# Kernel optimization log

Measured on AMD Instinct MI355X. Metric: run time of the kernel, lower is better.

The kernel has to match this reference:

```python
import jax, jax.numpy as jnp
import numpy as np

N, L, F, C, H, QK, Vd, Pq, Pv = 1, 512, 128, 64, 12, 32, 32, 8, 8


def _l2g(R, t, p):
    # p: (N,L,...,3) local -> global: R @ p + t
    o = jnp.einsum('nlij,nl...j->nl...i', R, p)
    return o + t.reshape(t.shape[0], t.shape[1], *((1,) * (p.ndim - 3)), 3)


def _g2l(R, t, q):
    # global -> local: R^T (q - t)
    d = q - t.reshape(t.shape[0], t.shape[1], *((1,) * (q.ndim - 3)), 3)
    return jnp.einsum('nlij,nl...i->nl...j', R, d)


def _ln(y, s, b, eps=1e-5):
    mu = y.mean(-1, keepdims=True)
    var = ((y - mu) ** 2).mean(-1, keepdims=True)
    return (y - mu) / jnp.sqrt(var + eps) * s + b


def setup_inputs() -> dict:
    key = jax.random.key(0)
    ks = jax.random.split(key, 16)
    sF = 1.0 / np.sqrt(F)
    sC = 1.0 / np.sqrt(C)
    cat = H * C + H * Vd + H * Pv * 3
    return {
        'R': jax.random.normal(ks[0], (N, L, 3, 3), jnp.float32),
        't': jax.random.normal(ks[1], (N, L, 3), jnp.float32),
        'x': jax.random.normal(ks[2], (N, L, F), jnp.float32),
        'z': jax.random.normal(ks[3], (N, L, L, C), jnp.float32),
        'mask': jnp.ones((N, L), dtype=bool),
        'Wq': jax.random.normal(ks[4], (F, H * QK), jnp.float32) * sF,
        'Wk': jax.random.normal(ks[5], (F, H * QK), jnp.float32) * sF,
        'Wpair': jax.random.normal(ks[6], (C, H), jnp.float32) * sC,
        'Wqp': jax.random.normal(ks[7], (F, H * Pq * 3), jnp.float32) * sF,
        'Wkp': jax.random.normal(ks[8], (F, H * Pq * 3), jnp.float32) * sF,
        'Wv': jax.random.normal(ks[9], (F, H * Vd), jnp.float32) * sF,
        'Wvp': jax.random.normal(ks[10], (F, H * Pv * 3), jnp.float32) * sF,
        'spatial_coef': jnp.full((1, 1, 1, H), np.log(np.e - 1.0), jnp.float32),
        'Wo': jax.random.normal(ks[11], (cat, F), jnp.float32) / np.sqrt(cat),
        'bo': jnp.zeros((F,), jnp.float32),
        'ln1_scale': jnp.ones((F,), jnp.float32),
        'ln1_offset': jnp.zeros((F,), jnp.float32),
        'W1': jax.random.normal(ks[12], (F, F), jnp.float32) * sF,
        'b1': jnp.zeros((F,), jnp.float32),
        'W2': jax.random.normal(ks[13], (F, F), jnp.float32) * sF,
        'b2': jnp.zeros((F,), jnp.float32),
        'W3': jax.random.normal(ks[14], (F, F), jnp.float32) * sF,
        'b3': jnp.zeros((F,), jnp.float32),
        'ln2_scale': jnp.ones((F,), jnp.float32),
        'ln2_offset': jnp.zeros((F,), jnp.float32),
    }


def reference(R, t, x, z, mask, Wq, Wk, Wpair, Wqp, Wkp, Wv, Wvp, spatial_coef,
              Wo, bo, ln1_scale, ln1_offset, W1, b1, W2, b2, W3, b3,
              ln2_scale, ln2_offset):
    # --- node logits ---
    q = (x @ Wq).reshape(N, L, H, QK)
    k = (x @ Wk).reshape(N, L, H, QK)
    logits_node = jnp.einsum('nihd,njhd->nijh', q, k) / np.float32(np.sqrt(QK))
    # --- pair logits ---
    logits_pair = z @ Wpair  # (N,L,L,H)
    # --- spatial logits ---
    qp = _l2g(R, t, (x @ Wqp).reshape(N, L, H * Pq, 3)).reshape(N, L, H, Pq * 3)
    kp = _l2g(R, t, (x @ Wkp).reshape(N, L, H * Pq, 3)).reshape(N, L, H, Pq * 3)
    q2 = (qp ** 2).sum(-1)  # (N,L,H)
    k2 = (kp ** 2).sum(-1)
    sum_sq_dist = q2[:, :, None] + k2[:, None] - 2.0 * jnp.einsum('nihd,njhd->nijh', qp, kp)
    gamma = jax.nn.softplus(spatial_coef)  # (1,1,1,H)
    logits_spatial = sum_sq_dist * (-gamma * np.float32(np.sqrt(2.0 / (9 * Pq))) / 2.0)
    # --- combine, mask, softmax ---
    logits = (logits_node + logits_pair + logits_spatial) * np.float32(np.sqrt(1.0 / 3.0))
    mask_pair = mask[:, :, None] & mask[:, None, :]  # (N,L,L)
    logits = jnp.where(mask_pair[..., None], logits, logits - 100000.0)
    alpha = jax.nn.softmax(logits, axis=2)
    alpha = jnp.where(mask[:, :, None, None], alpha, 0.0)
    # --- pair aggregation ---
    feat_p2n = jnp.einsum('nijh,nijc->nihc', alpha, z).reshape(N, L, H * C)
    # --- node aggregation ---
    v = (x @ Wv).reshape(N, L, H, Vd)
    feat_node = jnp.einsum('nijh,njhd->nihd', alpha, v).reshape(N, L, H * Vd)
    # --- spatial aggregation ---
    vp = _l2g(R, t, (x @ Wvp).reshape(N, L, H, Pv, 3))  # (N,L,H,Pv,3)
    aggr = jnp.einsum('nijh,njhpd->nihpd', alpha, vp)
    feat_points = _g2l(R, t, aggr)
    feat_spatial = feat_points.reshape(N, L, H * Pv * 3)
    # --- output transform + residual/LN + MLP ---
    feat_all = jnp.concatenate([feat_p2n, feat_node, feat_spatial], axis=-1) @ Wo + bo
    feat_all = jnp.where(mask[..., None], feat_all, 0.0)
    x1 = _ln(x + feat_all, ln1_scale, ln1_offset)
    h = jax.nn.relu(x1 @ W1 + b1)
    h = jax.nn.relu(h @ W2 + b2)
    mlp = h @ W3 + b3
    return _ln(x1 + mlp, ln2_scale, ln2_offset)
```

## Files before the change

kernel.cpp:

```cpp
#include <hip/hip_runtime.h>

#define PCOLS 2016

constexpr float INV_SQRT_QK = 0.17677669529663687f;
constexpr float S3          = 0.57735026918962576f;

#define FMA4(acc, s, b) { acc.x += (s)*(b).x; acc.y += (s)*(b).y; acc.z += (s)*(b).z; acc.w += (s)*(b).w; }
#define ADD4(acc, b)    { acc.x += (b).x; acc.y += (b).y; acc.z += (b).z; acc.w += (b).w; }

__global__ __launch_bounds__(384) void k1_gemm(
    const float* __restrict__ x,
    const float* __restrict__ Wq, const float* __restrict__ Wk,
    const float* __restrict__ Wqp, const float* __restrict__ Wkp,
    const float* __restrict__ Wv, const float* __restrict__ Wvp,
    float* __restrict__ proj) {
  int bt = blockIdx.x;
  int it = bt / 21, ot = bt % 21;
  int i0 = it * 64;
  int tid = threadIdx.x;
  __shared__ float xs[64 * 128];
  __shared__ float ws[128 * 96];
  const float* Wsec; int lofs, width;
  if (ot < 4)       { Wsec = Wq;  lofs = ot * 96;        width = 384; }
  else if (ot < 8)  { Wsec = Wk;  lofs = (ot - 4) * 96;  width = 384; }
  else if (ot < 11) { Wsec = Wqp; lofs = (ot - 8) * 96;  width = 288; }
  else if (ot < 14) { Wsec = Wkp; lofs = (ot - 11) * 96; width = 288; }
  else if (ot < 18) { Wsec = Wv;  lofs = (ot - 14) * 96; width = 384; }
  else              { Wsec = Wvp; lofs = (ot - 18) * 96; width = 288; }
  for (int g = tid; g < 2048; g += 384)
    *(float4*)(xs + (g >> 5) * 128 + (g & 31) * 4) =
      *(const float4*)(x + (size_t)(i0 + (g >> 5)) * 128 + (g & 31) * 4);
  for (int g = tid; g < 3072; g += 384) {
    int r = g / 24, u = g % 24;
    *(float4*)(ws + r * 96 + u * 4) = *(const float4*)(Wsec + (size_t)r * width + lofs + u * 4);
  }
  __syncthreads();
  int cg = tid % 24, tr = tid / 24;
  float4 acc0 = {0,0,0,0}, acc1 = {0,0,0,0}, acc2 = {0,0,0,0}, acc3 = {0,0,0,0};
  const float* x0 = xs + (tr * 4 + 0) * 128;
  const float* x1 = xs + (tr * 4 + 1) * 128;
  const float* x2 = xs + (tr * 4 + 2) * 128;
  const float* x3 = xs + (tr * 4 + 3) * 128;
  #pragma unroll 4
  for (int k = 0; k < 128; ++k) {
    float4 w = *(const float4*)(ws + k * 96 + cg * 4);
    FMA4(acc0, x0[k], w); FMA4(acc1, x1[k], w);
    FMA4(acc2, x2[k], w); FMA4(acc3, x3[k], w);
  }
  int gc = ot * 96 + cg * 4;
  *(float4*)(proj + (size_t)(i0 + tr * 4 + 0) * PCOLS + gc) = acc0;
  *(float4*)(proj + (size_t)(i0 + tr * 4 + 1) * PCOLS + gc) = acc1;
  *(float4*)(proj + (size_t)(i0 + tr * 4 + 2) * PCOLS + gc) = acc2;
  *(float4*)(proj + (size_t)(i0 + tr * 4 + 3) * PCOLS + gc) = acc3;
}

__global__ __launch_bounds__(256) void k1b_prep(
    const float* __restrict__ Rg, const float* __restrict__ tg, const float* __restrict__ sc,
    float* __restrict__ proj, float* __restrict__ Ac, float* __restrict__ BcT,
    float* __restrict__ a2, float* __restrict__ b2) {
  int j = blockIdx.x, tid = threadIdx.x;
  __shared__ float qk[1344];
  __shared__ float vps[288], Rs[9], ts[3], cf[12];
  float* pr = proj + (size_t)j * PCOLS;
  const float4* pr4 = (const float4*)pr;
  for (int g = tid; g < 336; g += 256) ((float4*)qk)[g] = pr4[g];
  for (int g = tid; g < 72; g += 256) ((float4*)vps)[g] = pr4[432 + g];
  if (tid < 9) Rs[tid] = Rg[j * 9 + tid];
  else if (tid < 12) ts[tid - 9] = tg[j * 3 + tid - 9];
  else if (tid < 24) cf[tid - 12] = -log1pf(__expf(sc[tid - 12])) * (1.0f / 12.0f);
  __syncthreads();
  for (int p = tid; p < 288; p += 256) {
    int sec = p / 96, m = p % 96;
    float* P = (sec == 0) ? qk + 768 : (sec == 1) ? qk + 1056 : vps;
    float* pp = P + m * 3;
    float p0 = pp[0], p1 = pp[1], p2 = pp[2];
    pp[0] = Rs[0]*p0 + Rs[1]*p1 + Rs[2]*p2 + ts[0];
    pp[1] = Rs[3]*p0 + Rs[4]*p1 + Rs[5]*p2 + ts[1];
    pp[2] = Rs[6]*p0 + Rs[7]*p1 + Rs[8]*p2 + ts[2];
  }
  __syncthreads();
  for (int g = tid; g < 72; g += 256) ((float4*)pr)[432 + g] = ((float4*)vps)[g];
  if (tid < 24) {
    int h = tid % 12;
    const float* s = (tid < 12) ? qk + 768 + h * 24 : qk + 1056 + h * 24;
    float a = 0.f;
    #pragma unroll
    for (int d = 0; d < 24; ++d) a += s[d] * s[d];
    float val = S3 * cf[h] * a;
    if (tid < 12) a2[h * 512 + j] = val; else b2[h * 512 + j] = val;
  }
  float s1 = S3 * INV_SQRT_QK;
  for (int o = tid; o < 672; o += 256) {
    int h = o / 56, d = o % 56;
    float s2 = -2.0f * S3 * cf[h];
    float aval = (d < 32) ? qk[h * 32 + d] * s1 : qk[768 + h * 24 + (d - 32)] * s2;
    float bval = (d < 32) ? qk[384 + h * 32 + d] : qk[1056 + h * 24 + (d - 32)];
    Ac[((size_t)h * 512 + j) * 56 + d] = aval;
    BcT[((size_t)h * 56 + d) * 512 + j] = bval;
  }
}

__global__ __launch_bounds__(256) void k2a_pair(
    const float* __restrict__ z, const float* __restrict__ Wpair,
    float* __restrict__ alphab) {
  int blk = blockIdx.x;
  int i = blk >> 2, j0 = (blk & 3) * 128;
  int tid = threadIdx.x;
  __shared__ float zt[128 * 68];
  __shared__ float wp[768];
  __shared__ float pl[12 * 128];
  if (tid < 192) ((float4*)wp)[tid] = ((const float4*)Wpair)[tid];
  const float4* zsrc = (const float4*)(z + ((size_t)i * 512 + j0) * 64);
  for (int g = tid; g < 2048; g += 256) {
    int row = g >> 4, c4 = g & 15;
    ((float4*)(zt + row * 68))[c4] = zsrc[row * 16 + c4];
  }
  __syncthreads();
  int jl = tid & 127, half = tid >> 7;
  float acc[12];
  #pragma unroll
  for (int h = 0; h < 12; ++h) acc[h] = 0.f;
  const float4* zr = (const float4*)(zt + jl * 68) + half * 8;
  #pragma unroll
  for (int c4 = 0; c4 < 8; ++c4) {
    float4 zv = zr[c4];
    const float* w0 = wp + (half * 8 + c4) * 48;
    #pragma unroll
    for (int h = 0; h < 12; ++h)
      acc[h] += zv.x * w0[h] + zv.y * w0[12 + h] + zv.z * w0[24 + h] + zv.w * w0[36 + h];
  }
  if (half == 1) {
    #pragma unroll
    for (int h = 0; h < 12; ++h) pl[h * 128 + jl] = acc[h];
  }
  __syncthreads();
  if (half == 0) {
    #pragma unroll
    for (int h = 0; h < 12; ++h)
      alphab[(size_t)h * 262144 + (size_t)i * 512 + j0 + jl] = (acc[h] + pl[h * 128 + jl]) * S3;
  }
}

__global__ __launch_bounds__(256) void k2b_logits(
    const float* __restrict__ Ac, const float* __restrict__ BcT,
    const float* __restrict__ a2, const float* __restrict__ b2,
    const float* __restrict__ proj, const float* __restrict__ Rg, const float* __restrict__ tg,
    float* __restrict__ alphab, float* __restrict__ featb) {
  int blk = blockIdx.x;
  int h = blk >> 5, i0 = (blk & 31) * 16;
  int tid = threadIdx.x;
  int ti = tid >> 5, tj = tid & 31;
  int r0 = 2 * ti;
  __shared__ float smem[12480];
  float* At  = smem;
  float* BtT = smem + 960;
  float* b2s = smem + 8352;
  float* a2s = smem + 8864;
  float* als = smem;
  float* Bt  = smem + 8256;
  float* ag  = smem + 12096;
  for (int g = tid; g < 224; g += 256) {
    int row = g / 14, u = g % 14;
    *(float4*)(At + row * 60 + u * 4) =
      *(const float4*)(Ac + ((size_t)h * 512 + i0 + row) * 56 + u * 4);
  }
  if (tid < 128) ((float4*)b2s)[tid] = ((const float4*)(b2 + h * 512))[tid];
  if (tid < 16) a2s[tid] = a2[h * 512 + i0 + tid];
  float lg[2][16];
  const size_t abase = (size_t)h * 262144;
  for (int jt = 0; jt < 4; ++jt) {
    int j0 = jt * 128;
    __syncthreads();
    for (int g = tid; g < 1792; g += 256) {
      int k = g >> 5, c4 = g & 31;
      *(float4*)(BtT + k * 132 + c4 * 4) =
        *(const float4*)(BcT + ((size_t)h * 56 + k) * 512 + j0 + c4 * 4);
    }
    __syncthreads();
    float acc[2][4] = {{0.f,0.f,0.f,0.f},{0.f,0.f,0.f,0.f}};
    #pragma unroll 8
    for (int k = 0; k < 56; ++k) {
      float a0 = At[r0 * 60 + k], a1 = At[(r0 + 1) * 60 + k];
      float2 bA = *(const float2*)(BtT + k * 132 + 2 * tj);
      float2 bB = *(const float2*)(BtT + k * 132 + 64 + 2 * tj);
      acc[0][0] += a0 * bA.x; acc[0][1] += a0 * bA.y; acc[0][2] += a0 * bB.x; acc[0][3] += a0 * bB.y;
      acc[1][0] += a1 * bA.x; acc[1][1] += a1 * bA.y; acc[1][2] += a1 * bB.x; acc[1][3] += a1 * bB.y;
    }
    #pragma unroll
    for (int r = 0; r < 2; ++r) {
      int ig = i0 + r0 + r;
      const float* prow = alphab + abase + (size_t)ig * 512 + j0;
      int c0 = 2 * tj, c1 = 64 + 2 * tj;
      float arr = a2s[r0 + r];
      lg[r][jt*4+0] = acc[r][0] + prow[c0]     + arr + b2s[j0 + c0];
      lg[r][jt*4+1] = acc[r][1] + prow[c0 + 1] + arr + b2s[j0 + c0 + 1];
      lg[r][jt*4+2] = acc[r][2] + prow[c1]     + arr + b2s[j0 + c1];
      lg[r][jt*4+3] = acc[r][3] + prow[c1 + 1] + arr + b2s[j0 + c1 + 1];
    }
  }
  __syncthreads();
  #pragma unroll
  for (int r = 0; r < 2; ++r) {
    float m = lg[r][0];
    #pragma unroll
    for (int u = 1; u < 16; ++u) m = fmaxf(m, lg[r][u]);
    #pragma unroll
    for (int s = 16; s > 0; s >>= 1) m = fmaxf(m, __shfl_xor(m, s));
    float ssum = 0.f;
    #pragma unroll
    for (int u = 0; u < 16; ++u) { lg[r][u] = __expf(lg[r][u] - m); ssum += lg[r][u]; }
    #pragma unroll
    for (int s = 16; s > 0; s >>= 1) ssum += __shfl_xor(ssum, s);
    float inv = 1.0f / ssum;
    int row = r0 + r;
    float* orow = alphab + abase + (size_t)(i0 + row) * 512;
    #pragma unroll
    for (int jt = 0; jt < 4; ++jt) {
      float2 vA = make_float2(lg[r][jt*4+0] * inv, lg[r][jt*4+1] * inv);
      float2 vB = make_float2(lg[r][jt*4+2] * inv, lg[r][jt*4+3] * inv);
      *(float2*)(orow + jt * 128 + 2 * tj)      = vA;
      *(float2*)(orow + jt * 128 + 64 + 2 * tj) = vB;
      *(float2*)(als + row * 516 + jt * 128 + 2 * tj)      = vA;
      *(float2*)(als + row * 516 + jt * 128 + 64 + 2 * tj) = vB;
    }
  }
  int cg2 = tid % 14, rg = tid / 14;
  int c0 = cg2 * 4;
  float4 acc4 = {0,0,0,0};
  for (int t8 = 0; t8 < 8; ++t8) {
    int j0 = t8 * 64;
    __syncthreads();
    for (int g = tid; g < 896; g += 256) {
      int row = g / 14, u = g % 14;
      const float* pr = proj + (size_t)(j0 + row) * PCOLS;
      float4 vv = (u < 8) ? *(const float4*)(&pr[1344 + h * 32 + u * 4])
                          : *(const float4*)(&pr[1728 + h * 24 + (u - 8) * 4]);
      int dst = (u < 8) ? u * 4 : 32 + (u - 8) * 4;
      *(float4*)(Bt + row * 60 + dst) = vv;
    }
    __syncthreads();
    if (rg < 16) {
      const float* arow = als + rg * 516 + j0;
      #pragma unroll 8
      for (int kk = 0; kk < 64; ++kk) {
        float a = arow[kk];
        float4 b = *(const float4*)(Bt + kk * 60 + c0);
        FMA4(acc4, a, b);
      }
    }
  }
  __syncthreads();
  if (rg < 16) {
    if (c0 < 32) {
      *(float4*)(&featb[(size_t)(i0 + rg) * 1440 + 768 + h * 32 + c0]) = acc4;
    } else {
      int cc = c0 - 32;
      ag[rg * 24 + cc + 0] = acc4.x; ag[rg * 24 + cc + 1] = acc4.y;
      ag[rg * 24 + cc + 2] = acc4.z; ag[rg * 24 + cc + 3] = acc4.w;
    }
  }
  __syncthreads();
  if (tid < 128) {
    int row = tid >> 3, p = tid & 7;
    const float* R  = Rg + (size_t)(i0 + row) * 9;
    const float* tt = tg + (size_t)(i0 + row) * 3;
    float d0 = ag[row * 24 + p * 3 + 0] - tt[0];
    float d1 = ag[row * 24 + p * 3 + 1] - tt[1];
    float d2 = ag[row * 24 + p * 3 + 2] - tt[2];
    float* o = featb + (size_t)(i0 + row) * 1440 + 1152 + h * 24 + p * 3;
    o[0] = R[0]*d0 + R[3]*d1 + R[6]*d2;
    o[1] = R[1]*d0 + R[4]*d1 + R[7]*d2;
    o[2] = R[2]*d0 + R[5]*d1 + R[8]*d2;
  }
}

__global__ __launch_bounds__(256) void k3a_p2n(
    const float* __restrict__ alphab, const float* __restrict__ z,
    float* __restrict__ featb) {
  int i = blockIdx.x, tid = threadIdx.x;
  __shared__ float al[12 * 516];
  __shared__ float zt[64 * 68];
  for (int g = tid; g < 1536; g += 256) {
    int row = g >> 7, c4 = g & 127;
    *(float4*)(al + row * 516 + c4 * 4) =
      *(const float4*)(alphab + (size_t)row * 262144 + (size_t)i * 512 + c4 * 4);
  }
  int h = tid >> 4, c4 = tid & 15;
  float4 acc = {0.f, 0.f, 0.f, 0.f};
  const float4* zsrc = (const float4*)(z + (size_t)i * 512 * 64);
  for (int t8 = 0; t8 < 8; ++t8) {
    __syncthreads();
    for (int g = tid; g < 1024; g += 256) {
      int row = g >> 4, cc = g & 15;
      *(float4*)(&zt[row * 68 + cc * 4]) = zsrc[(t8 * 64 + row) * 16 + cc];
    }
    __syncthreads();
    if (tid < 192) {
      const float* ar = al + h * 516 + t8 * 64;
      #pragma unroll
      for (int k4 = 0; k4 < 16; ++k4) {
        float4 a4 = *(const float4*)(&ar[k4 * 4]);
        float4 z0 = *(const float4*)(&zt[(k4*4+0) * 68 + c4 * 4]);
        float4 z1 = *(const float4*)(&zt[(k4*4+1) * 68 + c4 * 4]);
        float4 z2 = *(const float4*)(&zt[(k4*4+2) * 68 + c4 * 4]);
        float4 z3 = *(const float4*)(&zt[(k4*4+3) * 68 + c4 * 4]);
        FMA4(acc, a4.x, z0); FMA4(acc, a4.y, z1); FMA4(acc, a4.z, z2); FMA4(acc, a4.w, z3);
      }
    }
  }
  if (tid < 192)
    *(float4*)(&featb[(size_t)i * 1440 + h * 64 + c4 * 4]) = acc;
}

__global__ __launch_bounds__(512) void k4_mlp(
    const float* __restrict__ featb, const float* __restrict__ x,
    const float* __restrict__ Wo, const float* __restrict__ bo,
    const float* __restrict__ ln1s, const float* __restrict__ ln1o,
    const float* __restrict__ W1, const float* __restrict__ b1,
    const float* __restrict__ W2, const float* __restrict__ b2,
    const float* __restrict__ W3, const float* __restrict__ b3,
    const float* __restrict__ ln2s, const float* __restrict__ ln2o,
    float* __restrict__ out) {
  int i0 = blockIdx.x * 2;
  int tid = threadIdx.x;
  __shared__ float fs[2 * 1440];
  __shared__ float4 part4[16][2][32];
  __shared__ float stgA[2][128], stgB[2][128], stgC[2][128];
  for (int g = tid; g < 720; g += 512)
    ((float4*)fs)[g] = ((const float4*)(featb + (size_t)i0 * 1440))[g];
  __syncthreads();
  int q = tid >> 5, cg = tid & 31;
  {
    float4 a0 = {0,0,0,0}, a1 = {0,0,0,0};
    int cb = q * 90;
    const float* f0 = fs + cb, *f1 = fs + 1440 + cb;
    #pragma unroll 6
    for (int c = 0; c < 90; ++c) {
      float4 w = *((const float4*)(Wo + (size_t)(cb + c) * 128) + cg);
      FMA4(a0, f0[c], w);
      FMA4(a1, f1[c], w);
    }
    part4[q][0][cg] = a0;
    part4[q][1][cg] = a1;
  }
  __syncthreads();
  if (tid < 64) {
    int rr = tid >> 5, c = tid & 31;
    float4 s = part4[0][rr][c];
    #pragma unroll
    for (int k = 1; k < 16; ++k) ADD4(s, part4[k][rr][c]);
    float4 bo4 = ((const float4*)bo)[c];
    float4 xr4 = ((const float4*)(x + (size_t)(i0 + rr) * 128))[c];
    s.x += bo4.x + xr4.x; s.y += bo4.y + xr4.y; s.z += bo4.z + xr4.z; s.w += bo4.w + xr4.w;
    ((float4*)stgA[rr])[c] = s;
  }
  __syncthreads();
  int q2 = tid >> 7, col = tid & 127, rr = q2 & 1;
  float x1;
  {
    float y = stgA[rr][col];
    float s1 = 0.f, s2 = 0.f;
    #pragma unroll 8
    for (int c4 = 0; c4 < 32; ++c4) {
      float4 v = ((const float4*)stgA[rr])[c4];
      s1 += v.x + v.y + v.z + v.w;
      s2 += v.x*v.x + v.y*v.y + v.z*v.z + v.w*v.w;
    }
    float mu = s1 * (1.f / 128.f);
    float var = s2 * (1.f / 128.f) - mu * mu;
    x1 = (y - mu) * rsqrtf(var + 1e-5f) * ln1s[col] + ln1o[col];
  }
  __syncthreads();
  stgB[rr][col] = x1;
  __syncthreads();
  int sub = tid >> 5, rr1 = sub & 1, kq = sub >> 1;
  {
    float4 aa = {0,0,0,0};
    int c0 = kq * 16;
    #pragma unroll
    for (int c = 0; c < 16; ++c) {
      float4 w = *((const float4*)(W1 + (size_t)(c0 + c) * 128) + cg);
      FMA4(aa, stgB[rr1][c0 + c], w);
    }
    part4[sub][0][cg] = aa;
  }
  __syncthreads();
  if (tid < 64) {
    int r2 = tid >> 5, c = tid & 31;
    float4 s = part4[r2][0][c];
    #pragma unroll
    for (int k = 1; k < 8; ++k) ADD4(s, part4[k * 2 + r2][0][c]);
    float4 b4 = ((const float4*)b1)[c];
    s.x = fmaxf(s.x + b4.x, 0.f); s.y = fmaxf(s.y + b4.y, 0.f);
    s.z = fmaxf(s.z + b4.z, 0.f); s.w = fmaxf(s.w + b4.w, 0.f);
    ((float4*)stgA[r2])[c] = s;
  }
  __syncthreads();
  {
    float4 aa = {0,0,0,0};
    int c0 = kq * 16;
    #pragma unroll
    for (int c = 0; c < 16; ++c) {
      float4 w = *((const float4*)(W2 + (size_t)(c0 + c) * 128) + cg);
      FMA4(aa, stgA[rr1][c0 + c], w);
    }
    part4[sub][0][cg] = aa;
  }
  __syncthreads();
  if (tid < 64) {
    int r2 = tid >> 5, c = tid & 31;
    float4 s = part4[r2][0][c];
    #pragma unroll
    for (int k = 1; k < 8; ++k) ADD4(s, part4[k * 2 + r2][0][c]);
    float4 b4 = ((const float4*)b2)[c];
    s.x = fmaxf(s.x + b4.x, 0.f); s.y = fmaxf(s.y + b4.y, 0.f);
    s.z = fmaxf(s.z + b4.z, 0.f); s.w = fmaxf(s.w + b4.w, 0.f);
    ((float4*)stgC[r2])[c] = s;
  }
  __syncthreads();
  {
    float4 aa = {0,0,0,0};
    int c0 = kq * 16;
    #pragma unroll
    for (int c = 0; c < 16; ++c) {
      float4 w = *((const float4*)(W3 + (size_t)(c0 + c) * 128) + cg);
      FMA4(aa, stgC[rr1][c0 + c], w);
    }
    part4[sub][0][cg] = aa;
  }
  __syncthreads();
  if (tid < 64) {
    int r2 = tid >> 5, c = tid & 31;
    float4 s = part4[r2][0][c];
    #pragma unroll
    for (int k = 1; k < 8; ++k) ADD4(s, part4[k * 2 + r2][0][c]);
    float4 b4 = ((const float4*)b3)[c];
    s.x += b4.x; s.y += b4.y; s.z += b4.z; s.w += b4.w;
    ((float4*)stgA[r2])[c] = s;
  }
  __syncthreads();
  {
    float y2 = x1 + stgA[rr][col];
    stgC[rr][col] = y2;
    __syncthreads();
    float s1 = 0.f, s2 = 0.f;
    #pragma unroll 8
    for (int c4 = 0; c4 < 32; ++c4) {
      float4 v = ((const float4*)stgC[rr])[c4];
      s1 += v.x + v.y + v.z + v.w;
      s2 += v.x*v.x + v.y*v.y + v.z*v.z + v.w*v.w;
    }
    float mu = s1 * (1.f / 128.f);
    float var = s2 * (1.f / 128.f) - mu * mu;
    if (q2 < 2)
      out[(size_t)(i0 + rr) * 128 + col] = (y2 - mu) * rsqrtf(var + 1e-5f) * ln2s[col] + ln2o[col];
  }
}

extern "C" void kernel_launch(void* const* d_in, const int* in_sizes, int n_in,
                              void* d_out, int out_size, void* d_ws, size_t ws_size,
                              hipStream_t stream) {
  const float* Rg   = (const float*)d_in[0];
  const float* tg   = (const float*)d_in[1];
  const float* x    = (const float*)d_in[2];
  const float* z    = (const float*)d_in[3];
  const float* Wq   = (const float*)d_in[5];
  const float* Wk   = (const float*)d_in[6];
  const float* Wpair= (const float*)d_in[7];
  const float* Wqp  = (const float*)d_in[8];
  const float* Wkp  = (const float*)d_in[9];
  const float* Wv   = (const float*)d_in[10];
  const float* Wvp  = (const float*)d_in[11];
  const float* sc   = (const float*)d_in[12];
  const float* Wo   = (const float*)d_in[13];
  const float* bo   = (const float*)d_in[14];
  const float* ln1s = (const float*)d_in[15];
  const float* ln1o = (const float*)d_in[16];
  const float* W1   = (const float*)d_in[17];
  const float* b1   = (const float*)d_in[18];
  const float* W2   = (const float*)d_in[19];
  const float* b2   = (const float*)d_in[20];
  const float* W3   = (const float*)d_in[21];
  const float* b3   = (const float*)d_in[22];
  const float* ln2s = (const float*)d_in[23];
  const float* ln2o = (const float*)d_in[24];

  float* ws = (float*)d_ws;
  float* proj   = ws;
  float* Ac     = proj + 512 * 2016;
  float* BcT    = Ac + 344064;
  float* a2     = BcT + 344064;
  float* b2v    = a2 + 6144;
  float* alphab = b2v + 6144;
  float* featb  = alphab + 3145728;

  k1_gemm  <<<168, 384, 0, stream>>>(x, Wq, Wk, Wqp, Wkp, Wv, Wvp, proj);
  k1b_prep <<<512, 256, 0, stream>>>(Rg, tg, sc, proj, Ac, BcT, a2, b2v);
  k2a_pair <<<2048, 256, 0, stream>>>(z, Wpair, alphab);
  k2b_logits<<<384, 256, 0, stream>>>(Ac, BcT, a2, b2v, proj, Rg, tg, alphab, featb);
  k3a_p2n  <<<512, 256, 0, stream>>>(alphab, z, featb);
  k4_mlp   <<<256, 512, 0, stream>>>(featb, x, Wo, bo, ln1s, ln1o,
                                     W1, b1, W2, b2, W3, b3, ln2s, ln2o, (float*)d_out);
}
```

Measured before the change: 129.8 us.

## Double k2b_logits block size and split node/point aggregation across two halves

The k2b_logits kernel moves from 256 to 512 threads per block. In the logits phase each thread now computes 2 columns instead of 4 per tile, with the softmax reductions widened to the full 64-lane wavefront. In the aggregation phase the j range is split between two thread halves that each load their own B tile and accumulate partial sums, which are then combined through shared memory. The aim is more parallelism and latency hiding in this kernel, which launches only 384 blocks, at the cost of more shared memory per block and an extra reduction step.

```diff
diff --git a/kernel.cpp b/kernel.cpp
--- a/kernel.cpp
+++ b/kernel.cpp
@@ -141,7 +141,7 @@
   }
 }
 
-__global__ __launch_bounds__(256) void k2b_logits(
+__global__ __launch_bounds__(512) void k2b_logits(
     const float* __restrict__ Ac, const float* __restrict__ BcT,
     const float* __restrict__ a2, const float* __restrict__ b2,
     const float* __restrict__ proj, const float* __restrict__ Rg, const float* __restrict__ tg,
@@ -149,114 +149,118 @@
   int blk = blockIdx.x;
   int h = blk >> 5, i0 = (blk & 31) * 16;
   int tid = threadIdx.x;
-  int ti = tid >> 5, tj = tid & 31;
-  int r0 = 2 * ti;
-  __shared__ float smem[12480];
-  float* At  = smem;
-  float* BtT = smem + 960;
-  float* b2s = smem + 8352;
-  float* a2s = smem + 8864;
-  float* als = smem;
-  float* Bt  = smem + 8256;
-  float* ag  = smem + 12096;
-  for (int g = tid; g < 224; g += 256) {
+  __shared__ float smem[18736];
+  float* At   = smem;
+  float* BtT  = smem + 960;
+  float* b2s  = smem + 8352;
+  float* a2s  = smem + 8864;
+  float* als  = smem;
+  float* Bt2  = smem + 8880;
+  float4* part4 = (float4*)(smem + 16560);
+  float* ag   = smem + 18352;
+
+  for (int g = tid; g < 224; g += 512) {
     int row = g / 14, u = g % 14;
     *(float4*)(At + row * 60 + u * 4) =
       *(const float4*)(Ac + ((size_t)h * 512 + i0 + row) * 56 + u * 4);
   }
   if (tid < 128) ((float4*)b2s)[tid] = ((const float4*)(b2 + h * 512))[tid];
-  if (tid < 16) a2s[tid] = a2[h * 512 + i0 + tid];
-  float lg[2][16];
+  if (tid >= 128 && tid < 144) a2s[tid - 128] = a2[h * 512 + i0 + tid - 128];
+
+  int ti = tid >> 6, tj = tid & 63;
+  int r0 = 2 * ti;
+  float lg[2][8];
   const size_t abase = (size_t)h * 262144;
   for (int jt = 0; jt < 4; ++jt) {
     int j0 = jt * 128;
     __syncthreads();
-    for (int g = tid; g < 1792; g += 256) {
+    for (int g = tid; g < 1792; g += 512) {
       int k = g >> 5, c4 = g & 31;
       *(float4*)(BtT + k * 132 + c4 * 4) =
         *(const float4*)(BcT + ((size_t)h * 56 + k) * 512 + j0 + c4 * 4);
     }
     __syncthreads();
-    float acc[2][4] = {{0.f,0.f,0.f,0.f},{0.f,0.f,0.f,0.f}};
+    float a00 = 0.f, a01 = 0.f, a10 = 0.f, a11 = 0.f;
+    const float* At0 = At + r0 * 60;
     #pragma unroll 8
     for (int k = 0; k < 56; ++k) {
-      float a0 = At[r0 * 60 + k], a1 = At[(r0 + 1) * 60 + k];
-      float2 bA = *(const float2*)(BtT + k * 132 + 2 * tj);
-      float2 bB = *(const float2*)(BtT + k * 132 + 64 + 2 * tj);
-      acc[0][0] += a0 * bA.x; acc[0][1] += a0 * bA.y; acc[0][2] += a0 * bB.x; acc[0][3] += a0 * bB.y;
-      acc[1][0] += a1 * bA.x; acc[1][1] += a1 * bA.y; acc[1][2] += a1 * bB.x; acc[1][3] += a1 * bB.y;
-    }
-    #pragma unroll
-    for (int r = 0; r < 2; ++r) {
-      int ig = i0 + r0 + r;
-      const float* prow = alphab + abase + (size_t)ig * 512 + j0;
-      int c0 = 2 * tj, c1 = 64 + 2 * tj;
-      float arr = a2s[r0 + r];
-      lg[r][jt*4+0] = acc[r][0] + prow[c0]     + arr + b2s[j0 + c0];
-      lg[r][jt*4+1] = acc[r][1] + prow[c0 + 1] + arr + b2s[j0 + c0 + 1];
-      lg[r][jt*4+2] = acc[r][2] + prow[c1]     + arr + b2s[j0 + c1];
-      lg[r][jt*4+3] = acc[r][3] + prow[c1 + 1] + arr + b2s[j0 + c1 + 1];
-    }
+      float a0 = At0[k], a1 = At0[60 + k];
+      float2 b = *(const float2*)(BtT + k * 132 + 2 * tj);
+      a00 += a0 * b.x; a01 += a0 * b.y;
+      a10 += a1 * b.x; a11 += a1 * b.y;
+    }
+    int c0 = j0 + 2 * tj;
+    const float* prow0 = alphab + abase + (size_t)(i0 + r0) * 512;
+    const float* prow1 = prow0 + 512;
+    float bb0 = b2s[c0], bb1 = b2s[c0 + 1];
+    lg[0][jt*2+0] = a00 + prow0[c0]     + a2s[r0]     + bb0;
+    lg[0][jt*2+1] = a01 + prow0[c0 + 1] + a2s[r0]     + bb1;
+    lg[1][jt*2+0] = a10 + prow1[c0]     + a2s[r0 + 1] + bb0;
+    lg[1][jt*2+1] = a11 + prow1[c0 + 1] + a2s[r0 + 1] + bb1;
   }
   __syncthreads();
   #pragma unroll
   for (int r = 0; r < 2; ++r) {
     float m = lg[r][0];
     #pragma unroll
-    for (int u = 1; u < 16; ++u) m = fmaxf(m, lg[r][u]);
-    #pragma unroll
-    for (int s = 16; s > 0; s >>= 1) m = fmaxf(m, __shfl_xor(m, s));
+    for (int u = 1; u < 8; ++u) m = fmaxf(m, lg[r][u]);
+    #pragma unroll
+    for (int s = 32; s > 0; s >>= 1) m = fmaxf(m, __shfl_xor(m, s));
     float ssum = 0.f;
     #pragma unroll
-    for (int u = 0; u < 16; ++u) { lg[r][u] = __expf(lg[r][u] - m); ssum += lg[r][u]; }
-    #pragma unroll
-    for (int s = 16; s > 0; s >>= 1) ssum += __shfl_xor(ssum, s);
+    for (int u = 0; u < 8; ++u) { lg[r][u] = __expf(lg[r][u] - m); ssum += lg[r][u]; }
+    #pragma unroll
+    for (int s = 32; s > 0; s >>= 1) ssum += __shfl_xor(ssum, s);
     float inv = 1.0f / ssum;
     int row = r0 + r;
     float* orow = alphab + abase + (size_t)(i0 + row) * 512;
     #pragma unroll
     for (int jt = 0; jt < 4; ++jt) {
-      float2 vA = make_float2(lg[r][jt*4+0] * inv, lg[r][jt*4+1] * inv);
-      float2 vB = make_float2(lg[r][jt*4+2] * inv, lg[r][jt*4+3] * inv);
-      *(float2*)(orow + jt * 128 + 2 * tj)      = vA;
-      *(float2*)(orow + jt * 128 + 64 + 2 * tj) = vB;
-      *(float2*)(als + row * 516 + jt * 128 + 2 * tj)      = vA;
-      *(float2*)(als + row * 516 + jt * 128 + 64 + 2 * tj) = vB;
-    }
-  }
-  int cg2 = tid % 14, rg = tid / 14;
-  int c0 = cg2 * 4;
+      float2 v = make_float2(lg[r][jt*2+0] * inv, lg[r][jt*2+1] * inv);
+      *(float2*)(orow + jt * 128 + 2 * tj) = v;
+      *(float2*)(als + row * 516 + jt * 128 + 2 * tj) = v;
+    }
+  }
+  int half = tid / 224, rem = tid % 224;
+  int rg = rem / 14, cgp = rem % 14;
+  int c0p = cgp * 4;
   float4 acc4 = {0,0,0,0};
-  for (int t8 = 0; t8 < 8; ++t8) {
-    int j0 = t8 * 64;
-    __syncthreads();
-    for (int g = tid; g < 896; g += 256) {
-      int row = g / 14, u = g % 14;
-      const float* pr = proj + (size_t)(j0 + row) * PCOLS;
+  for (int tt = 0; tt < 4; ++tt) {
+    __syncthreads();
+    for (int g = tid; g < 1792; g += 512) {
+      int hh = g / 896, gg = g % 896;
+      int row = gg / 14, u = gg % 14;
+      const float* pr = proj + (size_t)((tt + 4 * hh) * 64 + row) * PCOLS;
       float4 vv = (u < 8) ? *(const float4*)(&pr[1344 + h * 32 + u * 4])
                           : *(const float4*)(&pr[1728 + h * 24 + (u - 8) * 4]);
       int dst = (u < 8) ? u * 4 : 32 + (u - 8) * 4;
-      *(float4*)(Bt + row * 60 + dst) = vv;
-    }
-    __syncthreads();
-    if (rg < 16) {
-      const float* arow = als + rg * 516 + j0;
+      *(float4*)(Bt2 + hh * 3840 + row * 60 + dst) = vv;
+    }
+    __syncthreads();
+    if (tid < 448) {
+      const float* arow = als + rg * 516 + (tt + 4 * half) * 64;
+      const float* bt = Bt2 + half * 3840;
       #pragma unroll 8
       for (int kk = 0; kk < 64; ++kk) {
         float a = arow[kk];
-        float4 b = *(const float4*)(Bt + kk * 60 + c0);
+        float4 b = *(const float4*)(bt + kk * 60 + c0p);
         FMA4(acc4, a, b);
       }
     }
   }
   __syncthreads();
-  if (rg < 16) {
-    if (c0 < 32) {
-      *(float4*)(&featb[(size_t)(i0 + rg) * 1440 + 768 + h * 32 + c0]) = acc4;
+  if (tid < 448) part4[half * 224 + rg * 14 + cgp] = acc4;
+  __syncthreads();
+  if (tid < 224) {
+    float4 s = part4[rem];
+    float4 s2 = part4[224 + rem];
+    ADD4(s, s2);
+    if (c0p < 32) {
+      *(float4*)(&featb[(size_t)(i0 + rg) * 1440 + 768 + h * 32 + c0p]) = s;
     } else {
-      int cc = c0 - 32;
-      ag[rg * 24 + cc + 0] = acc4.x; ag[rg * 24 + cc + 1] = acc4.y;
-      ag[rg * 24 + cc + 2] = acc4.z; ag[rg * 24 + cc + 3] = acc4.w;
+      int cc = c0p - 32;
+      ag[rg * 24 + cc + 0] = s.x; ag[rg * 24 + cc + 1] = s.y;
+      ag[rg * 24 + cc + 2] = s.z; ag[rg * 24 + cc + 3] = s.w;
     }
   }
   __syncthreads();
@@ -497,7 +501,7 @@
   k1_gemm  <<<168, 384, 0, stream>>>(x, Wq, Wk, Wqp, Wkp, Wv, Wvp, proj);
   k1b_prep <<<512, 256, 0, stream>>>(Rg, tg, sc, proj, Ac, BcT, a2, b2v);
   k2a_pair <<<2048, 256, 0, stream>>>(z, Wpair, alphab);
-  k2b_logits<<<384, 256, 0, stream>>>(Ac, BcT, a2, b2v, proj, Rg, tg, alphab, featb);
+  k2b_logits<<<384, 512, 0, stream>>>(Ac, BcT, a2, b2v, proj, Rg, tg, alphab, featb);
   k3a_p2n  <<<512, 256, 0, stream>>>(alphab, z, featb);
   k4_mlp   <<<256, 512, 0, stream>>>(featb, x, Wo, bo, ln1s, ln1o,
                                      W1, b1, W2, b2, W3, b3, ln2s, ln2o, (float*)d_out);
```

After: 120.1 us. 7.4% less time.
